# Kernel tuning notes

Hardware: AMD Instinct MI355X
Metric: run time of the kernel (lower is better)

The kernel has to match this reference:

```python
import jax, jax.numpy as jnp
import numpy as np

N_NODES = 100000
N_EDGES = 1600000
IN_CH, HID_CH, OUT_CH = 128, 128, 64


def setup_inputs() -> dict:
    key = jax.random.key(0)
    k1, k2, k3, k4 = jax.random.split(key, 4)
    x = jax.random.normal(k1, (N_NODES, IN_CH), dtype=jnp.float32)
    edge_index = jax.random.randint(k2, (2, N_EDGES), 0, N_NODES, dtype=jnp.int32)
    # Glorot-style init for GCNConv linear weights, zeros for bias (PyG default)
    s1 = (6.0 / (IN_CH + HID_CH)) ** 0.5
    s2 = (6.0 / (HID_CH + OUT_CH)) ** 0.5
    W1 = jax.random.uniform(k3, (IN_CH, HID_CH), jnp.float32, -s1, s1)
    W2 = jax.random.uniform(k4, (HID_CH, OUT_CH), jnp.float32, -s2, s2)
    b1 = jnp.zeros((HID_CH,), jnp.float32)
    b2 = jnp.zeros((OUT_CH,), jnp.float32)
    return {"x": x, "edge_index": edge_index, "W1": W1, "b1": b1, "W2": W2, "b2": b2}


def reference(x, edge_index, W1, b1, W2, b2):
    N = x.shape[0]
    # gcn_norm with add_self_loops=True, edge_weight=None -> ones
    loop = jnp.arange(N, dtype=edge_index.dtype)
    row = jnp.concatenate([edge_index[0], loop])  # source nodes
    col = jnp.concatenate([edge_index[1], loop])  # target nodes
    ew = jnp.ones(row.shape[0], dtype=x.dtype)
    deg = jax.ops.segment_sum(ew, col, num_segments=N)           # in-degree incl. self-loops
    dis = jnp.where(deg > 0, jax.lax.rsqrt(deg), 0.0)            # deg^{-1/2}, inf -> 0
    norm = dis[row] * ew * dis[col]                              # per-edge normalization

    def gcn_conv(h, W, b):
        h = h @ W                                                # [N, d_out]
        msg = h[row] * norm[:, None]                             # gather + scale [E+N, d_out]
        return jax.ops.segment_sum(msg, col, num_segments=N) + b  # scatter-add

    h = jax.nn.relu(gcn_conv(x, W1, b1))
    # F.dropout with training=False is identity (eval mode reference)
    return gcn_conv(h, W2, b2)
```

## Files before the change

### kernel.cpp

```cpp
#include <hip/hip_runtime.h>
#include <hip/hip_fp16.h>
#include <type_traits>


constexpr int BSH = 9;
constexpr int BNODES = 1 << BSH;
constexpr int CHUNK = 4096;
constexpr int CAP = 12288;

typedef __attribute__((ext_vector_type(8))) _Float16 half8;
typedef __attribute__((ext_vector_type(4))) float f32x4;

__global__ __launch_bounds__(256) void zero_kernel(int* __restrict__ p, int n) {
    int i = blockIdx.x * 256 + threadIdx.x;
    if (i < n) p[i] = 0;
}

__global__ __launch_bounds__(256) void hist_kernel(const int* __restrict__ col,
                                                   int* __restrict__ bhist,
                                                   int E, int NB) {
    __shared__ int lh[256];
    int t = threadIdx.x;
    lh[t] = 0;
    __syncthreads();
    for (int i = blockIdx.x * 256 + t; i < E; i += gridDim.x * 256)
        atomicAdd(&lh[col[i] >> BSH], 1);
    __syncthreads();
    if (t < NB && lh[t]) atomicAdd(&bhist[t], lh[t]);
}

__global__ __launch_bounds__(256) void bbase_scan_kernel(const int* __restrict__ bhist,
                                                         int* __restrict__ bbase,
                                                         int* __restrict__ bcur, int NB) {
    __shared__ int s[256];
    int t = threadIdx.x;
    int v = (t < NB) ? bhist[t] : 0;
    s[t] = v;
    __syncthreads();
    for (int d = 1; d < 256; d <<= 1) {
        int u = (t >= d) ? s[t - d] : 0;
        __syncthreads();
        s[t] += u;
        __syncthreads();
    }
    if (t < NB) { bbase[t] = s[t] - v; bcur[t] = s[t] - v; }
    if (t == NB - 1) bbase[NB] = s[t];
}

__global__ __launch_bounds__(256) void bucket_scatter_kernel(const int* __restrict__ row,
                                                             const int* __restrict__ col,
                                                             int* __restrict__ bcur,
                                                             int2* __restrict__ pairs,
                                                             int E, int NB) {
    __shared__ int2 sp[CHUNK];
    __shared__ int lhist[256], lofs[256], lcur[256], gbase[256];
    int t = threadIdx.x;
    int start = blockIdx.x * CHUNK;
    int cnt = min(CHUNK, E - start);
    lhist[t] = 0;
    __syncthreads();
    for (int i = t; i < cnt; i += 256)
        atomicAdd(&lhist[col[start + i] >> BSH], 1);
    __syncthreads();
    int v = lhist[t];
    lofs[t] = v;
    __syncthreads();
    for (int d = 1; d < 256; d <<= 1) {
        int u = (t >= d) ? lofs[t - d] : 0;
        __syncthreads();
        lofs[t] += u;
        __syncthreads();
    }
    int excl = lofs[t] - v;
    lofs[t] = excl;
    lcur[t] = excl;
    if (t < NB && v > 0) gbase[t] = atomicAdd(&bcur[t], v);
    __syncthreads();
    for (int i = t; i < cnt; i += 256) {
        int c = col[start + i];
        int s = row[start + i];
        int lp = atomicAdd(&lcur[c >> BSH], 1);
        sp[lp] = make_int2(s, c);
    }
    __syncthreads();
    for (int i = t; i < cnt; i += 256) {
        int2 pr = sp[i];
        int b = pr.y >> BSH;
        pairs[gbase[b] + (i - lofs[b])] = pr;
    }
}

__global__ __launch_bounds__(256) void place_kernel(const int2* __restrict__ pairs,
                                                    const int* __restrict__ bbase,
                                                    int* __restrict__ off,
                                                    float* __restrict__ dis,
                                                    int* __restrict__ csr, int N, int NB) {
    __shared__ int lhist[BNODES], lexcl[BNODES], lcur2[BNODES];
    __shared__ int sscan[256];
    __shared__ int lout[CAP];
    int b = blockIdx.x;
    int t = threadIdx.x;
    int n0 = b << BSH;
    int n1 = min(n0 + BNODES, N);
    int nn = n1 - n0;
    int base = bbase[b];
    int cnt = bbase[b + 1] - base;
    lhist[2 * t] = 0;
    lhist[2 * t + 1] = 0;
    __syncthreads();
    for (int i = t; i < cnt; i += 256)
        atomicAdd(&lhist[pairs[base + i].y - n0], 1);
    __syncthreads();
    int a0 = lhist[2 * t], a1 = lhist[2 * t + 1];
    int ps = a0 + a1;
    sscan[t] = ps;
    __syncthreads();
    for (int d = 1; d < 256; d <<= 1) {
        int u = (t >= d) ? sscan[t - d] : 0;
        __syncthreads();
        sscan[t] += u;
        __syncthreads();
    }
    int pexcl = sscan[t] - ps;
    lexcl[2 * t] = pexcl;
    lexcl[2 * t + 1] = pexcl + a0;
    lcur2[2 * t] = pexcl;
    lcur2[2 * t + 1] = pexcl + a0;
    __syncthreads();
    for (int i = t; i < nn; i += 256) {
        off[n0 + i] = base + lexcl[i];
        dis[n0 + i] = rsqrtf((float)(lhist[i] + 1));
    }
    if (b == NB - 1 && t == 0) off[N] = base + cnt;
    for (int i = t; i < cnt; i += 256) {
        int2 pr = pairs[base + i];
        int lp = atomicAdd(&lcur2[pr.y - n0], 1);
        if (lp < CAP) lout[lp] = pr.x;
        else csr[base + lp] = pr.x;
    }
    __syncthreads();
    int staged = min(cnt, CAP);
    for (int i = t; i < staged; i += 256) csr[base + i] = lout[i];
}

template<int TN>
__global__ __launch_bounds__(256) void wtrans_kernel(const float* __restrict__ W,
                                                     _Float16* __restrict__ WT) {
    int i = blockIdx.x * 256 + threadIdx.x;
    if (i < TN * 128) {
        int n = i % TN, k = i / TN;
        WT[n * 128 + k] = (_Float16)W[k * TN + n];
    }
}

template<int TN, typename TI>
__global__ __launch_bounds__(256) void gemm_kernel(const TI* __restrict__ X,
                                                   const _Float16* __restrict__ WT,
                                                   const float* __restrict__ dis,
                                                   __half* __restrict__ Y, int M) {
    constexpr int K = 128;
    constexpr int NT = TN / 16;
    constexpr int LDA = 136;
    __shared__ _Float16 Ah[64 * LDA];
    __shared__ _Float16 Bh[TN * LDA];
    int tid = threadIdx.x;
    int row0 = blockIdx.x * 64;

#pragma unroll
    for (int j = 0; j < TN / 16; ++j) {
        int lin = tid + j * 256;
        int n = lin >> 4, kq = lin & 15;
        *(uint4*)&Bh[n * LDA + kq * 8] = *(const uint4*)(WT + n * 128 + kq * 8);
    }
    if constexpr (std::is_same<TI, float>::value) {
#pragma unroll
        for (int j = 0; j < 8; ++j) {
            int lin = tid + j * 256;
            int r = lin >> 5, kq = lin & 31;
            int row = row0 + r;
            float4 v = make_float4(0.f, 0.f, 0.f, 0.f);
            if (row < M) v = *(const float4*)(X + (size_t)row * K + kq * 4);
            __half2 h01 = __float22half2_rn(make_float2(v.x, v.y));
            __half2 h23 = __float22half2_rn(make_float2(v.z, v.w));
            uint2 u = make_uint2(*reinterpret_cast<unsigned*>(&h01),
                                 *reinterpret_cast<unsigned*>(&h23));
            *(uint2*)&Ah[r * LDA + kq * 4] = u;
        }
    } else {
#pragma unroll
        for (int j = 0; j < 4; ++j) {
            int lin = tid + j * 256;
            int r = lin >> 4, kq = lin & 15;
            int row = row0 + r;
            uint4 u = make_uint4(0, 0, 0, 0);
            if (row < M) u = *(const uint4*)(X + (size_t)row * K + kq * 8);
            *(uint4*)&Ah[r * LDA + kq * 8] = u;
        }
    }
    __syncthreads();

    int w = tid >> 6, l = tid & 63;
    int lr = l & 15, kg = l >> 4;
    f32x4 acc[NT];
#pragma unroll
    for (int nt = 0; nt < NT; ++nt) acc[nt] = (f32x4){0.f, 0.f, 0.f, 0.f};

    const _Float16* arow = &Ah[(w * 16 + lr) * LDA + kg * 8];
#pragma unroll
    for (int ks = 0; ks < 4; ++ks) {
        half8 af = *(const half8*)(arow + ks * 32);
#pragma unroll
        for (int nt = 0; nt < NT; ++nt) {
            half8 bf = *(const half8*)(&Bh[(nt * 16 + lr) * LDA + ks * 32 + kg * 8]);
            acc[nt] = __builtin_amdgcn_mfma_f32_16x16x32_f16(af, bf, acc[nt], 0, 0, 0);
        }
    }

#pragma unroll
    for (int j = 0; j < 4; ++j) {
        int grow = row0 + w * 16 + kg * 4 + j;
        if (grow < M) {
            float sc = dis[grow];
#pragma unroll
            for (int nt = 0; nt < NT; ++nt)
                Y[(size_t)grow * TN + nt * 16 + lr] = __float2half_rn(sc * acc[nt][j]);
        }
    }
}

template<int C, bool RELU, typename TOUT>
__global__ __launch_bounds__(256) void agg_kernel(const __half* __restrict__ Hs,
                                                  const int* __restrict__ off,
                                                  const int* __restrict__ src,
                                                  const float* __restrict__ dis,
                                                  const float* __restrict__ bias,
                                                  TOUT* __restrict__ out, int N) {
    constexpr int HPL = C / 32;
    int node = blockIdx.x * 8 + (threadIdx.x >> 5);
    if (node >= N) return;
    int lane = threadIdx.x & 31;
    float dv = dis[node];
    float acc[HPL];
    {
        const __half* hp = Hs + (size_t)node * C + lane * HPL;
        if constexpr (HPL == 4) {
            uint2 u = *(const uint2*)hp;
            float2 f0 = __half22float2(*reinterpret_cast<__half2*>(&u.x));
            float2 f1 = __half22float2(*reinterpret_cast<__half2*>(&u.y));
            acc[0] = f0.x; acc[1] = f0.y; acc[2] = f1.x; acc[3] = f1.y;
        } else {
            float2 f0 = __half22float2(*(const __half2*)hp);
            acc[0] = f0.x; acc[1] = f0.y;
        }
    }
    int e0 = off[node], e1 = off[node + 1];
    for (int e = e0; e < e1; e += 8) {
        int s[8];
        float w[8];
#pragma unroll
        for (int k = 0; k < 8; ++k) {
            int idx = e + k;
            bool ok = idx < e1;
            s[k] = src[ok ? idx : e1 - 1];
            w[k] = ok ? 1.0f : 0.0f;
        }
        if constexpr (HPL == 4) {
            uint2 v[8];
#pragma unroll
            for (int k = 0; k < 8; ++k)
                v[k] = *(const uint2*)(Hs + (size_t)s[k] * C + lane * 4);
#pragma unroll
            for (int k = 0; k < 8; ++k) {
                float2 f0 = __half22float2(*reinterpret_cast<__half2*>(&v[k].x));
                float2 f1 = __half22float2(*reinterpret_cast<__half2*>(&v[k].y));
                acc[0] = fmaf(w[k], f0.x, acc[0]);
                acc[1] = fmaf(w[k], f0.y, acc[1]);
                acc[2] = fmaf(w[k], f1.x, acc[2]);
                acc[3] = fmaf(w[k], f1.y, acc[3]);
            }
        } else {
            unsigned int v[8];
#pragma unroll
            for (int k = 0; k < 8; ++k)
                v[k] = *(const unsigned int*)(Hs + (size_t)s[k] * C + lane * 2);
#pragma unroll
            for (int k = 0; k < 8; ++k) {
                float2 f0 = __half22float2(*reinterpret_cast<__half2*>(&v[k]));
                acc[0] = fmaf(w[k], f0.x, acc[0]);
                acc[1] = fmaf(w[k], f0.y, acc[1]);
            }
        }
    }
    float r[HPL];
#pragma unroll
    for (int f = 0; f < HPL; ++f) {
        r[f] = fmaf(dv, acc[f], bias[lane * HPL + f]);
        if (RELU) r[f] = fmaxf(r[f], 0.0f);
    }
    if constexpr (std::is_same<TOUT, __half>::value) {
        __half2 hv[HPL / 2];
#pragma unroll
        for (int q = 0; q < HPL / 2; ++q)
            hv[q] = __float22half2_rn(make_float2(r[2 * q], r[2 * q + 1]));
        if constexpr (HPL == 4)
            *(uint2*)(out + (size_t)node * C + lane * 4) = *reinterpret_cast<uint2*>(&hv[0]);
        else
            *(unsigned int*)(out + (size_t)node * C + lane * 2) =
                *reinterpret_cast<unsigned int*>(&hv[0]);
    } else {
        if constexpr (HPL == 4) {
            *(float4*)(out + (size_t)node * C + lane * 4) =
                make_float4(r[0], r[1], r[2], r[3]);
        } else {
            *(float2*)(out + (size_t)node * C + lane * 2) = make_float2(r[0], r[1]);
        }
    }
}

extern "C" void kernel_launch(void* const* d_in, const int* in_sizes, int n_in,
                              void* d_out, int out_size, void* d_ws, size_t ws_size,
                              hipStream_t stream) {
    const float* x  = (const float*)d_in[0];
    const int*   ei = (const int*)d_in[1];
    const float* W1 = (const float*)d_in[2];
    const float* b1 = (const float*)d_in[3];
    const float* W2 = (const float*)d_in[4];
    const float* b2 = (const float*)d_in[5];
    float* out = (float*)d_out;

    int N = in_sizes[0] / 128;
    int E = in_sizes[1] / 2;
    const int* row = ei;
    const int* col = ei + E;
    int NB = (N + BNODES - 1) >> BSH;

    char* ws = (char*)d_ws;
    size_t o = 0;
    auto alloc = [&](size_t bytes) -> void* {
        void* p = ws + o;
        o = (o + bytes + 255) & ~(size_t)255;
        return p;
    };
    int*      bhist = (int*)alloc((size_t)(NB + 1) * 4);
    int*      bbase = (int*)alloc((size_t)(NB + 1) * 4);
    int*      bcur  = (int*)alloc((size_t)NB * 4);
    int*      off   = (int*)alloc((size_t)(N + 1) * 4);
    float*    dis   = (float*)alloc((size_t)N * 4);
    int*      csr   = (int*)alloc((size_t)E * 4);
    _Float16* w1t   = (_Float16*)alloc(128 * 128 * 2);
    _Float16* w2t   = (_Float16*)alloc(64 * 128 * 2);
    __half*   xw    = (__half*)alloc((size_t)N * 128 * 2);
    __half*   h     = (__half*)alloc((size_t)N * 128 * 2);
    int2*     pairs = (int2*)alloc((size_t)E * 8);
    __half*   hw2   = xw;

    zero_kernel<<<1, 256, 0, stream>>>(bhist, NB);
    wtrans_kernel<128><<<64, 256, 0, stream>>>(W1, w1t);
    wtrans_kernel<64><<<32, 256, 0, stream>>>(W2, w2t);
    hist_kernel<<<1024, 256, 0, stream>>>(col, bhist, E, NB);
    bbase_scan_kernel<<<1, 256, 0, stream>>>(bhist, bbase, bcur, NB);
    bucket_scatter_kernel<<<(E + CHUNK - 1) / CHUNK, 256, 0, stream>>>(row, col, bcur,
                                                                       pairs, E, NB);
    place_kernel<<<NB, 256, 0, stream>>>(pairs, bbase, off, dis, csr, N, NB);

    gemm_kernel<128, float><<<(N + 63) / 64, 256, 0, stream>>>(x, w1t, dis, xw, N);
    agg_kernel<128, true, __half><<<(N + 7) / 8, 256, 0, stream>>>(xw, off, csr, dis,
                                                                   b1, h, N);
    gemm_kernel<64, __half><<<(N + 63) / 64, 256, 0, stream>>>(h, w2t, dis, hw2, N);
    agg_kernel<64, false, float><<<(N + 7) / 8, 256, 0, stream>>>(hw2, off, csr, dis,
                                                                  b2, out, N);
}
```

Baseline: 205.3 us.

## Use 16 lanes per node with wider gathers and a zero sentinel row

The aggregation kernel now assigns 16 lanes per node instead of 32, so each lane loads 16-byte (C=128) or 8-byte (C=64) vectors per neighbour row. Padding edges now index an extra zero row at position N instead of re-reading the last edge with a zero weight, which removes the per-edge multiply. Two small kernels zero that sentinel row before each aggregation. The intent is fewer, wider memory transactions per gathered row and more nodes per block, at the cost of more registers per lane and two extra tiny launches.

New measurement: 204.3 us. Within noise of the previous version (-0.5%).

```diff
diff --git a/kernel.cpp b/kernel.cpp
--- a/kernel.cpp
+++ b/kernel.cpp
@@ -14,6 +14,11 @@
 __global__ __launch_bounds__(256) void zero_kernel(int* __restrict__ p, int n) {
     int i = blockIdx.x * 256 + threadIdx.x;
     if (i < n) p[i] = 0;
+}
+
+__global__ __launch_bounds__(256) void zero_halfs_kernel(__half* __restrict__ p, int n) {
+    int i = threadIdx.x;
+    if (i < n) reinterpret_cast<unsigned short*>(p)[i] = 0;
 }
 
 __global__ __launch_bounds__(256) void hist_kernel(const int* __restrict__ col,
@@ -235,59 +240,45 @@
                                                   const float* __restrict__ dis,
                                                   const float* __restrict__ bias,
                                                   TOUT* __restrict__ out, int N) {
-    constexpr int HPL = C / 32;
-    int node = blockIdx.x * 8 + (threadIdx.x >> 5);
+    constexpr int HPL = C / 16;
+    constexpr int NV = HPL / 2;
+    using VT = std::conditional_t<HPL == 8, uint4, uint2>;
+    int node = blockIdx.x * 16 + (threadIdx.x >> 4);
     if (node >= N) return;
-    int lane = threadIdx.x & 31;
+    int lane = threadIdx.x & 15;
+    const __half* hbase = Hs + lane * HPL;
     float dv = dis[node];
     float acc[HPL];
     {
-        const __half* hp = Hs + (size_t)node * C + lane * HPL;
-        if constexpr (HPL == 4) {
-            uint2 u = *(const uint2*)hp;
-            float2 f0 = __half22float2(*reinterpret_cast<__half2*>(&u.x));
-            float2 f1 = __half22float2(*reinterpret_cast<__half2*>(&u.y));
-            acc[0] = f0.x; acc[1] = f0.y; acc[2] = f1.x; acc[3] = f1.y;
-        } else {
-            float2 f0 = __half22float2(*(const __half2*)hp);
-            acc[0] = f0.x; acc[1] = f0.y;
+        VT sv = *(const VT*)(hbase + (size_t)node * C);
+        const unsigned int* u = reinterpret_cast<const unsigned int*>(&sv);
+#pragma unroll
+        for (int q = 0; q < NV; ++q) {
+            float2 f = __half22float2(*reinterpret_cast<const __half2*>(&u[q]));
+            acc[2 * q] = f.x;
+            acc[2 * q + 1] = f.y;
         }
     }
     int e0 = off[node], e1 = off[node + 1];
     for (int e = e0; e < e1; e += 8) {
         int s[8];
-        float w[8];
 #pragma unroll
         for (int k = 0; k < 8; ++k) {
             int idx = e + k;
-            bool ok = idx < e1;
-            s[k] = src[ok ? idx : e1 - 1];
-            w[k] = ok ? 1.0f : 0.0f;
-        }
-        if constexpr (HPL == 4) {
-            uint2 v[8];
-#pragma unroll
-            for (int k = 0; k < 8; ++k)
-                v[k] = *(const uint2*)(Hs + (size_t)s[k] * C + lane * 4);
-#pragma unroll
-            for (int k = 0; k < 8; ++k) {
-                float2 f0 = __half22float2(*reinterpret_cast<__half2*>(&v[k].x));
-                float2 f1 = __half22float2(*reinterpret_cast<__half2*>(&v[k].y));
-                acc[0] = fmaf(w[k], f0.x, acc[0]);
-                acc[1] = fmaf(w[k], f0.y, acc[1]);
-                acc[2] = fmaf(w[k], f1.x, acc[2]);
-                acc[3] = fmaf(w[k], f1.y, acc[3]);
-            }
-        } else {
-            unsigned int v[8];
-#pragma unroll
-            for (int k = 0; k < 8; ++k)
-                v[k] = *(const unsigned int*)(Hs + (size_t)s[k] * C + lane * 2);
-#pragma unroll
-            for (int k = 0; k < 8; ++k) {
-                float2 f0 = __half22float2(*reinterpret_cast<__half2*>(&v[k]));
-                acc[0] = fmaf(w[k], f0.x, acc[0]);
-                acc[1] = fmaf(w[k], f0.y, acc[1]);
+            s[k] = (idx < e1) ? src[idx] : N;
+        }
+        VT v[8];
+#pragma unroll
+        for (int k = 0; k < 8; ++k)
+            v[k] = *(const VT*)(hbase + (size_t)s[k] * C);
+#pragma unroll
+        for (int k = 0; k < 8; ++k) {
+            const unsigned int* u = reinterpret_cast<const unsigned int*>(&v[k]);
+#pragma unroll
+            for (int q = 0; q < NV; ++q) {
+                float2 f = __half22float2(*reinterpret_cast<const __half2*>(&u[q]));
+                acc[2 * q] += f.x;
+                acc[2 * q + 1] += f.y;
             }
         }
     }
@@ -298,21 +289,20 @@
         if (RELU) r[f] = fmaxf(r[f], 0.0f);
     }
     if constexpr (std::is_same<TOUT, __half>::value) {
-        __half2 hv[HPL / 2];
-#pragma unroll
-        for (int q = 0; q < HPL / 2; ++q)
+        __half2 hv[NV];
+#pragma unroll
+        for (int q = 0; q < NV; ++q)
             hv[q] = __float22half2_rn(make_float2(r[2 * q], r[2 * q + 1]));
-        if constexpr (HPL == 4)
-            *(uint2*)(out + (size_t)node * C + lane * 4) = *reinterpret_cast<uint2*>(&hv[0]);
-        else
-            *(unsigned int*)(out + (size_t)node * C + lane * 2) =
-                *reinterpret_cast<unsigned int*>(&hv[0]);
+        *(VT*)(out + (size_t)node * C + lane * HPL) = *reinterpret_cast<VT*>(&hv[0]);
     } else {
-        if constexpr (HPL == 4) {
+        if constexpr (HPL == 8) {
+            *(float4*)(out + (size_t)node * C + lane * 8) =
+                make_float4(r[0], r[1], r[2], r[3]);
+            *(float4*)(out + (size_t)node * C + lane * 8 + 4) =
+                make_float4(r[4], r[5], r[6], r[7]);
+        } else {
             *(float4*)(out + (size_t)node * C + lane * 4) =
                 make_float4(r[0], r[1], r[2], r[3]);
-        } else {
-            *(float2*)(out + (size_t)node * C + lane * 2) = make_float2(r[0], r[1]);
         }
     }
 }
@@ -349,8 +339,8 @@
     int*      csr   = (int*)alloc((size_t)E * 4);
     _Float16* w1t   = (_Float16*)alloc(128 * 128 * 2);
     _Float16* w2t   = (_Float16*)alloc(64 * 128 * 2);
-    __half*   xw    = (__half*)alloc((size_t)N * 128 * 2);
-    __half*   h     = (__half*)alloc((size_t)N * 128 * 2);
+    __half*   xw    = (__half*)alloc(((size_t)N * 128 + 128) * 2);
+    __half*   h     = (__half*)alloc(((size_t)N * 128 + 128) * 2);
     int2*     pairs = (int2*)alloc((size_t)E * 8);
     __half*   hw2   = xw;
 
@@ -364,9 +354,11 @@
     place_kernel<<<NB, 256, 0, stream>>>(pairs, bbase, off, dis, csr, N, NB);
 
     gemm_kernel<128, float><<<(N + 63) / 64, 256, 0, stream>>>(x, w1t, dis, xw, N);
-    agg_kernel<128, true, __half><<<(N + 7) / 8, 256, 0, stream>>>(xw, off, csr, dis,
-                                                                   b1, h, N);
+    zero_halfs_kernel<<<1, 256, 0, stream>>>(xw + (size_t)N * 128, 128);
+    agg_kernel<128, true, __half><<<(N + 15) / 16, 256, 0, stream>>>(xw, off, csr, dis,
+                                                                     b1, h, N);
     gemm_kernel<64, __half><<<(N + 63) / 64, 256, 0, stream>>>(h, w2t, dis, hw2, N);
-    agg_kernel<64, false, float><<<(N + 7) / 8, 256, 0, stream>>>(hw2, off, csr, dis,
-                                                                  b2, out, N);
-}
+    zero_halfs_kernel<<<1, 256, 0, stream>>>(hw2 + (size_t)N * 64, 64);
+    agg_kernel<64, false, float><<<(N + 15) / 16, 256, 0, stream>>>(hw2, off, csr, dis,
+                                                                    b2, out, N);
+}
```
